# Kernel optimization log

Hardware: AMD Instinct MI355X
Metric: run time of the kernel (lower is better)

Reference implementation:

```python
import jax, jax.numpy as jnp
import numpy as np

IN_SIZE = 784
Z_DIM = 128
K_DIM = 8192
BATCH = 16384
ENC_HIDDEN = [512, 256]          # EncoderMLP default
DEC_SIZES = [Z_DIM, 256, 512, 784]  # DecoderMLP default: [latent, *hidden]


def _linear(x, w, b):
    return x @ w + b


def find_nearest(query, target):
    # Faithful to: sqrt(sum((Q-T)^2, -1)).min(1)[1]; sqrt is monotone so
    # argmin of squared distance is identical. Computed via the GEMM
    # expansion instead of materializing the (N,K,D) broadcast tensor.
    q2 = jnp.sum(query * query, axis=1, keepdims=True)        # [N,1]
    t2 = jnp.sum(target * target, axis=1)                     # [K]
    d2 = q2 - 2.0 * (query @ target.T) + t2[None, :]          # [N,K]
    idx = jnp.argmin(d2, axis=1)
    return target[idx]


def setup_inputs() -> dict:
    key = jax.random.key(0)
    ks = jax.random.split(key, 16)
    s = 0.02
    inp = {"X": jax.random.uniform(ks[0], (BATCH, 1, 28, 28), dtype=jnp.float32)}
    # Encoder: 784 -> 512 -> 256 (mlp blocks, ReLU) -> 128 (plain Linear)
    enc_sizes = [IN_SIZE] + ENC_HIDDEN + [Z_DIM]
    for i, (din, dout) in enumerate(zip(enc_sizes, enc_sizes[1:]), 1):
        inp[f"enc_w{i}"] = s * jax.random.normal(ks[i], (din, dout), dtype=jnp.float32)
        inp[f"enc_b{i}"] = jnp.zeros((dout,), dtype=jnp.float32)
    # Codebook
    inp["codebook"] = jax.random.normal(ks[8], (K_DIM, Z_DIM), dtype=jnp.float32)
    # Decoder: 128 -> 256 -> 512 -> 784 (mlp blocks, ReLU) + sigmoid out
    for i, (din, dout) in enumerate(zip(DEC_SIZES, DEC_SIZES[1:]), 1):
        inp[f"dec_w{i}"] = s * jax.random.normal(ks[8 + i], (din, dout), dtype=jnp.float32)
        inp[f"dec_b{i}"] = jnp.zeros((dout,), dtype=jnp.float32)
    return inp


def reference(X, enc_w1, enc_b1, enc_w2, enc_b2, enc_w3, enc_b3, codebook,
              dec_w1, dec_b1, dec_w2, dec_b2, dec_w3, dec_b3):
    x = X.reshape(-1, IN_SIZE)
    # Encoder (mlp_block = Linear+ReLU, final layer plain Linear)
    h = jax.nn.relu(_linear(x, enc_w1, enc_b1))
    h = jax.nn.relu(_linear(h, enc_w2, enc_b2))
    z_enc = _linear(h, enc_w3, enc_b3)                         # [N, Z]
    # Nearest codebook vector for each encoding
    z_dec = find_nearest(z_enc, codebook)                      # [N, Z]
    # Decoder
    d = jax.nn.relu(_linear(z_dec, dec_w1, dec_b1))
    d = jax.nn.relu(_linear(d, dec_w2, dec_b2))
    d = jax.nn.relu(_linear(d, dec_w3, dec_b3))
    x_recon = jax.nn.sigmoid(d).reshape(-1, 1, 28, 28)
    # Nearest encoding for each codebook vector (for embedding loss)
    z_enc_for_embd = find_nearest(codebook, z_enc)             # [K, Z]
    return (x_recon, z_enc, z_dec, z_enc_for_embd)
```

## Files before the change

kernel.cpp:

```cpp
#include <hip/hip_runtime.h>
#include <math.h>

using u16 = unsigned short;
using u32 = unsigned int;
using u64 = unsigned long long;

typedef __bf16 bf16x8 __attribute__((ext_vector_type(8)));
typedef short  s16x8  __attribute__((ext_vector_type(8)));
typedef float  f32x4  __attribute__((ext_vector_type(4)));

__device__ __forceinline__ float b2f(u16 u){
  union { u32 i; float f; } x; x.i = ((u32)u) << 16; return x.f;
}
__device__ __forceinline__ u16 f2b(float f){
  union { float f; u32 i; } x; x.f = f;
  u32 i = x.i;
  u32 r = (i + 0x7fffu + ((i >> 16) & 1u)) >> 16;
  return (u16)r;
}
__device__ __forceinline__ f32x4 mfma16(s16x8 a, s16x8 b, f32x4 c){
  return __builtin_amdgcn_mfma_f32_16x16x32_bf16(
      __builtin_bit_cast(bf16x8, a), __builtin_bit_cast(bf16x8, b), c, 0, 0, 0);
}
__device__ __forceinline__ u64 shfl_xor_u64(u64 v, int m){
  int lo = __shfl_xor((int)(u32)v, m);
  int hi = __shfl_xor((int)(u32)(v >> 32), m);
  return ((u64)(u32)hi << 32) | (u32)lo;
}
__device__ __forceinline__ u64 umin64(u64 a, u64 b){ return a < b ? a : b; }
__device__ __forceinline__ u64 packmin(float v, int idx){
  u32 b = __float_as_uint(v);
  b = (b & 0x80000000u) ? ~b : (b | 0x80000000u);
  return ((u64)b << 32) | (u32)idx;
}
__device__ __forceinline__ void gload16(const void* g, void* l){
  __builtin_amdgcn_global_load_lds(
      (const __attribute__((address_space(1))) unsigned int*)g,
      (__attribute__((address_space(3))) unsigned int*)l, 16, 0, 0);
}

__global__ __launch_bounds__(256) void canary_k(float* out, float code){
  out[threadIdx.x] = code;
}

__global__ __launch_bounds__(256) void prep_weights(
    const float* __restrict__ w1, const float* __restrict__ w2, const float* __restrict__ w3,
    const float* __restrict__ dw1, const float* __restrict__ dw2, const float* __restrict__ dw3,
    const float* __restrict__ cb,
    u16* __restrict__ o1h, u16* __restrict__ o1l, u16* __restrict__ o2h, u16* __restrict__ o2l,
    u16* __restrict__ o3h, u16* __restrict__ o3l, u16* __restrict__ o4h, u16* __restrict__ o4l,
    u16* __restrict__ o5h, u16* __restrict__ o5l, u16* __restrict__ o6h, u16* __restrict__ o6l,
    u16* __restrict__ cbh, u16* __restrict__ cbl)
{
  size_t o = (size_t)blockIdx.x * 256 + threadIdx.x;
  if (o >= 1155072){
    size_t e = o - 1155072;
    if (e >= 1048576) return;
    float v = cb[e];
    u16 h = f2b(v);
    cbh[e] = h;
    cbl[e] = f2b(v - b2f(h));
    return;
  }
  const float* src; u16 *hi, *lo; int K, N, Kp; size_t base;
  if      (o <  425984){ src=w1;  hi=o1h; lo=o1l; K=784; N=512; Kp=832; base=0; }
  else if (o <  557056){ src=w2;  hi=o2h; lo=o2l; K=512; N=256; Kp=512; base=425984; }
  else if (o <  589824){ src=w3;  hi=o3h; lo=o3l; K=256; N=128; Kp=256; base=557056; }
  else if (o <  622592){ src=dw1; hi=o4h; lo=o4l; K=128; N=256; Kp=128; base=589824; }
  else if (o <  753664){ src=dw2; hi=o5h; lo=o5l; K=256; N=512; Kp=256; base=622592; }
  else                 { src=dw3; hi=o6h; lo=o6l; K=512; N=784; Kp=512; base=753664; }
  size_t e = o - base;
  int n = (int)(e / Kp), kp = (int)(e % Kp);
  u16 h = 0, l = 0;
  if (kp < K){
    float v = src[(size_t)kp * N + n];
    h = f2b(v);
    l = f2b(v - b2f(h));
  }
  hi[e] = h; lo[e] = l;
}

__device__ __forceinline__ void norm_row(const float* __restrict__ src, float* __restrict__ dst){
  const float4* r = (const float4*)src;
  float s = 0.f;
  for (int k = 0; k < 32; k++){
    float4 p = r[k];
    s += p.x * p.x + p.y * p.y + p.z * p.z + p.w * p.w;
  }
  *dst = s;
}

struct __align__(16) SmemGemm {
  u16 Ah[128][72];
  u16 Al[128][72];
  u16 Bh[128][72];
  u16 Bl[128][72];
};

template<int ACT, int OUTP>
__device__ __forceinline__ void gemm_body(
    SmemGemm& sm,
    const float* __restrict__ A, const u16* __restrict__ B0, const u16* __restrict__ B1,
    const float* __restrict__ bias, float* __restrict__ Cf,
    u16* __restrict__ P0, u16* __restrict__ P1,
    int Astr, int KLIM, int Kp, int KT, int N, int nRowsB, int bx, int by)
{
  const int tid = threadIdx.x;
  const int m0 = by * 128, n0 = bx * 128;
  const int wave = tid >> 6, lane = tid & 63;
  const int wm = (wave >> 1) * 64, wn = (wave & 1) * 64;
  const int quad = lane >> 4, l15 = lane & 15;
  f32x4 acc[4][4] = {};

  for (int kt = 0; kt < KT; ++kt){
    const int kb = kt * 64;
    #pragma unroll
    for (int c = 0; c < 8; c++){
      int idx = c * 256 + tid;
      int r = idx >> 4, c4 = (idx & 15) * 4;
      float4 v = make_float4(0.f, 0.f, 0.f, 0.f);
      if (kb + c4 < KLIM)
        v = *(const float4*)(A + (size_t)(m0 + r) * Astr + kb + c4);
      ushort4 h, l;
      h.x = f2b(v.x); l.x = f2b(v.x - b2f(h.x));
      h.y = f2b(v.y); l.y = f2b(v.y - b2f(h.y));
      h.z = f2b(v.z); l.z = f2b(v.z - b2f(h.z));
      h.w = f2b(v.w); l.w = f2b(v.w - b2f(h.w));
      *(ushort4*)&sm.Ah[r][c4] = h;
      *(ushort4*)&sm.Al[r][c4] = l;
    }
    #pragma unroll
    for (int c = 0; c < 4; c++){
      int idx = c * 256 + tid;
      int r = idx >> 3, col = (idx & 7) * 8;
      int rb = n0 + r; rb = rb < nRowsB ? rb : nRowsB - 1;
      *(uint4*)&sm.Bh[r][col] = *(const uint4*)(B0 + (size_t)rb * Kp + kb + col);
      *(uint4*)&sm.Bl[r][col] = *(const uint4*)(B1 + (size_t)rb * Kp + kb + col);
    }
    __syncthreads();
    #pragma unroll
    for (int kh = 0; kh < 2; ++kh){
      s16x8 ah[4], al[4], bh[4], bl[4];
      #pragma unroll
      for (int t4 = 0; t4 < 4; t4++){
        ah[t4] = *(const s16x8*)&sm.Ah[wm + t4 * 16 + l15][kh * 32 + quad * 8];
        al[t4] = *(const s16x8*)&sm.Al[wm + t4 * 16 + l15][kh * 32 + quad * 8];
        bh[t4] = *(const s16x8*)&sm.Bh[wn + t4 * 16 + l15][kh * 32 + quad * 8];
        bl[t4] = *(const s16x8*)&sm.Bl[wn + t4 * 16 + l15][kh * 32 + quad * 8];
      }
      #pragma unroll
      for (int mt = 0; mt < 4; mt++)
        #pragma unroll
        for (int nt = 0; nt < 4; nt++){
          acc[mt][nt] = mfma16(ah[mt], bh[nt], acc[mt][nt]);
          acc[mt][nt] = mfma16(ah[mt], bl[nt], acc[mt][nt]);
          acc[mt][nt] = mfma16(al[mt], bh[nt], acc[mt][nt]);
        }
    }
    __syncthreads();
  }

  float bvs[4]; int cols[4];
  #pragma unroll
  for (int nt = 0; nt < 4; nt++){
    int cN = n0 + wn + nt * 16 + l15;
    cols[nt] = cN;
    int cc = cN < N ? cN : N - 1;
    bvs[nt] = bias[cc];
  }
  #pragma unroll
  for (int mt = 0; mt < 4; mt++){
    int rbase = m0 + wm + mt * 16 + quad * 4;
    #pragma unroll
    for (int nt = 0; nt < 4; nt++){
      if (cols[nt] < N){
        #pragma unroll
        for (int r = 0; r < 4; r++){
          float v = acc[mt][nt][r] + bvs[nt];
          if (ACT >= 1) v = v > 0.f ? v : 0.f;
          if (ACT == 2) v = 1.f / (1.f + expf(-v));
          size_t off = (size_t)(rbase + r) * N + cols[nt];
          if (OUTP == 2){
            P0[off] = f2b(v);
          } else {
            Cf[off] = v;
            if (OUTP == 1){
              u16 h = f2b(v);
              P0[off] = h;
              P1[off] = f2b(v - b2f(h));
            }
          }
        }
      }
    }
  }
}

template<int ACT, int OUTP>
__global__ __launch_bounds__(256, 2) void gemm_k(
    const float* __restrict__ A, const u16* __restrict__ B0, const u16* __restrict__ B1,
    const float* __restrict__ bias, float* __restrict__ Cf,
    u16* __restrict__ P0, u16* __restrict__ P1,
    int Astr, int KLIM, int Kp, int KT, int N, int nRowsB)
{
  __shared__ SmemGemm sm;
  gemm_body<ACT, OUTP>(sm, A, B0, B1, bias, Cf, P0, P1, Astr, KLIM, Kp, KT, N, nRowsB,
                       blockIdx.x, blockIdx.y);
}

__global__ __launch_bounds__(256, 2) void fused1(
    const float* __restrict__ X,  const u16* __restrict__ W1h, const u16* __restrict__ W1l,
    const float* __restrict__ b1, float* __restrict__ h1,
    const float* __restrict__ cb, const u16* __restrict__ D1h, const u16* __restrict__ D1l,
    const float* __restrict__ db1, float* __restrict__ g1, float* __restrict__ t2f)
{
  __shared__ SmemGemm sm;
  int bid = blockIdx.x;
  if (bid < 512){
    gemm_body<1,0>(sm, X, W1h, W1l, b1, h1, nullptr, nullptr, 784, 784, 832, 13, 512, 512,
                   bid & 3, bid >> 2);
  } else if (bid < 640){
    int b = bid - 512;
    gemm_body<1,0>(sm, cb, D1h, D1l, db1, g1, nullptr, nullptr, 128, 128, 128, 2, 256, 256,
                   b & 1, b >> 1);
  } else {
    int r = (bid - 640) * 256 + threadIdx.x;
    norm_row(cb + (size_t)r * 128, t2f + r);
  }
}

__global__ __launch_bounds__(256, 2) void fused2(
    const float* __restrict__ h1, const u16* __restrict__ W2h, const u16* __restrict__ W2l,
    const float* __restrict__ b2, float* __restrict__ h2,
    const float* __restrict__ g1, const u16* __restrict__ D2h, const u16* __restrict__ D2l,
    const float* __restrict__ db2, float* __restrict__ g2)
{
  __shared__ SmemGemm sm;
  int bid = blockIdx.x;
  if (bid < 256){
    gemm_body<1,0>(sm, h1, W2h, W2l, b2, h2, nullptr, nullptr, 512, 512, 512, 8, 256, 256,
                   bid & 1, bid >> 1);
  } else {
    int b = bid - 256;
    gemm_body<1,0>(sm, g1, D2h, D2l, db2, g2, nullptr, nullptr, 256, 256, 256, 4, 512, 512,
                   b & 3, b >> 2);
  }
}

struct __align__(16) DistSmem {
  u16 smem[2][16384];
  u64 colbuf[4][128];
  u64 sRow[2][128];
  float q2s[128];
};

__device__ __forceinline__ void dist_body(
    DistSmem& sm,
    const u16* __restrict__ Zh, const u16* __restrict__ Zl,
    const u16* __restrict__ Bh, const u16* __restrict__ Bl,
    const float* __restrict__ zenc, const float* __restrict__ t2,
    u64* __restrict__ rowp, u64* __restrict__ colp, int strip, int iblk)
{
  const int tid = threadIdx.x;
  const int i0 = iblk * 128;
  const int wave = tid >> 6, lane = tid & 63;
  const int wm = (wave >> 1) * 32, wn = (wave & 1) * 64;
  const int quad = lane >> 4, l15 = lane & 15;

  const int swz = (l15 & 7) << 4;
  const int cof0 = (((quad << 4)     ) ^ swz) >> 1;
  const int cof1 = (((quad << 4) | 64) ^ swz) >> 1;

  if (tid < 128){
    norm_row(zenc + (size_t)(i0 + tid) * 128, &sm.q2s[tid]);
  }

  s16x8 zh[2][2][2], zl[2][2][2];
  #pragma unroll
  for (int kb = 0; kb < 2; kb++)
    #pragma unroll
    for (int kh = 0; kh < 2; kh++)
      #pragma unroll
      for (int mt = 0; mt < 2; mt++){
        size_t off = (size_t)(i0 + wm + mt * 16 + l15) * 128 + kb * 64 + kh * 32 + quad * 8;
        zh[kb][kh][mt] = *(const s16x8*)(Zh + off);
        zl[kb][kh][mt] = *(const s16x8*)(Zl + off);
      }

  #define STAGE(jt_, kb_, buf_) {                                              \
    size_t jb = (size_t)(strip * 2048 + (jt_) * 128) * 128 + (kb_) * 64;       \
    _Pragma("unroll")                                                          \
    for (int c = 0; c < 2; c++){                                               \
      int ci = c * 512 + tid;                                                  \
      int row = ci >> 3;                                                       \
      size_t g = jb + (size_t)row * 128 + (size_t)(((ci & 7) ^ (row & 7)) * 8);\
      u16* lp = &sm.smem[buf_][ci * 8];                                        \
      gload16(Bh + g, lp);                                                     \
      gload16(Bl + g, lp + 8192);                                              \
    }                                                                          \
  }

  #define COMPUTE(buf_, kb_) {                                                 \
    __builtin_amdgcn_s_setprio(1);                                             \
    _Pragma("unroll")                                                          \
    for (int kh = 0; kh < 2; kh++){                                            \
      const int cof = kh ? cof1 : cof0;                                        \
      s16x8 bh[4], bl[4];                                                      \
      _Pragma("unroll")                                                        \
      for (int nt = 0; nt < 4; nt++){                                          \
        int off = (wn + nt * 16 + l15) * 64 + cof;                             \
        bh[nt] = *(const s16x8*)&sm.smem[buf_][off];                           \
        bl[nt] = *(const s16x8*)&sm.smem[buf_][8192 + off];                    \
      }                                                                        \
      _Pragma("unroll")                                                        \
      for (int mt = 0; mt < 2; mt++)                                           \
        _Pragma("unroll")                                                      \
        for (int nt = 0; nt < 4; nt++){                                        \
          acc[mt][nt] = mfma16(zh[kb_][kh][mt], bh[nt], acc[mt][nt]);          \
          acc[mt][nt] = mfma16(zh[kb_][kh][mt], bl[nt], acc[mt][nt]);          \
          acc[mt][nt] = mfma16(zl[kb_][kh][mt], bh[nt], acc[mt][nt]);          \
          acc[mt][nt] = mfma16(zl[kb_][kh][mt], bl[nt], acc[mt][nt]);          \
        }                                                                      \
    }                                                                          \
    __builtin_amdgcn_s_setprio(0);                                             \
  }

  STAGE(0, 0, 0);

  asm volatile("s_waitcnt lgkmcnt(0)" ::: "memory");
  __builtin_amdgcn_s_barrier();

  float qv[2][4];
  #pragma unroll
  for (int mt = 0; mt < 2; mt++)
    #pragma unroll
    for (int r = 0; r < 4; r++)
      qv[mt][r] = sm.q2s[wm + mt * 16 + quad * 4 + r];

  u64 rowm[2][4];
  #pragma unroll
  for (int mt = 0; mt < 2; mt++)
    #pragma unroll
    for (int r = 0; r < 4; r++) rowm[mt][r] = ~0ULL;

  #pragma unroll 1
  for (int jt = 0; jt < 16; ++jt){
    const int j0 = strip * 2048 + jt * 128;
    float t2v[4]; int gj[4];
    #pragma unroll
    for (int nt = 0; nt < 4; nt++){
      gj[nt] = j0 + wn + nt * 16 + l15;
      t2v[nt] = t2[gj[nt]];
    }
    f32x4 acc[2][4] = {};

    STAGE(jt, 1, 1);
    asm volatile("s_waitcnt vmcnt(8)" ::: "memory");
    __builtin_amdgcn_s_barrier();
    COMPUTE(0, 0)
    __builtin_amdgcn_s_barrier();
    if (jt < 15){
      STAGE(jt + 1, 0, 0);
      asm volatile("s_waitcnt vmcnt(4)" ::: "memory");
    } else {
      asm volatile("s_waitcnt vmcnt(0)" ::: "memory");
    }
    __builtin_amdgcn_s_barrier();
    COMPUTE(1, 1)

    #pragma unroll
    for (int mt = 0; mt < 2; mt++){
      #pragma unroll
      for (int r = 0; r < 4; r++){
        float qq = qv[mt][r];
        float rbest = (qq - 2.f * acc[mt][0][r]) + t2v[0];
        int   ridx  = gj[0];
        #pragma unroll
        for (int nt = 1; nt < 4; nt++){
          float v = (qq - 2.f * acc[mt][nt][r]) + t2v[nt];
          if (v < rbest){ rbest = v; ridx = gj[nt]; }
        }
        rowm[mt][r] = umin64(rowm[mt][r], packmin(rbest, ridx));
      }
    }
    #pragma unroll
    for (int nt = 0; nt < 4; nt++){
      float cbest = 3.4e38f; int cidx = 0;
      #pragma unroll
      for (int mt = 0; mt < 2; mt++){
        #pragma unroll
        for (int r = 0; r < 4; r++){
          float vc = (t2v[nt] - 2.f * acc[mt][nt][r]) + qv[mt][r];
          if (vc < cbest){ cbest = vc; cidx = i0 + wm + mt * 16 + quad * 4 + r; }
        }
      }
      u64 p = packmin(cbest, cidx);
      p = umin64(p, shfl_xor_u64(p, 16));
      p = umin64(p, shfl_xor_u64(p, 32));
      if (quad == 0)
        sm.colbuf[wave >> 1][wn + nt * 16 + l15] = p;
    }
    __builtin_amdgcn_s_barrier();
    if (tid < 128){
      u64 p = umin64(umin64(sm.colbuf[0][tid], sm.colbuf[1][tid]),
                     umin64(sm.colbuf[2][tid], sm.colbuf[3][tid]));
      colp[(size_t)iblk * 8192 + j0 + tid] = p;
    }
  }
  #undef STAGE
  #undef COMPUTE

  #pragma unroll
  for (int mt = 0; mt < 2; mt++)
    #pragma unroll
    for (int r = 0; r < 4; r++){
      u64 p = rowm[mt][r];
      p = umin64(p, shfl_xor_u64(p, 1));
      p = umin64(p, shfl_xor_u64(p, 2));
      p = umin64(p, shfl_xor_u64(p, 4));
      p = umin64(p, shfl_xor_u64(p, 8));
      rowm[mt][r] = p;
    }
  if (l15 == 0){
    #pragma unroll
    for (int mt = 0; mt < 2; mt++)
      #pragma unroll
      for (int r = 0; r < 4; r++)
        sm.sRow[wave & 1][wm + mt * 16 + quad * 4 + r] = rowm[mt][r];
  }
  __syncthreads();
  if (tid < 128)
    rowp[(size_t)strip * 16384 + i0 + tid] = umin64(sm.sRow[0][tid], sm.sRow[1][tid]);
}

union SmemF4 { SmemGemm g; DistSmem d; };

__global__ __launch_bounds__(512, 2) void fused_dd(
    const u16* __restrict__ Zh, const u16* __restrict__ Zl,
    const u16* __restrict__ Bh, const u16* __restrict__ Bl,
    const float* __restrict__ zenc, const float* __restrict__ t2,
    u64* __restrict__ rowp, u64* __restrict__ colp,
    const float* __restrict__ g2, const u16* __restrict__ D3h, const u16* __restrict__ D3l,
    const float* __restrict__ db3, u16* __restrict__ xdecb)
{
  __shared__ SmemF4 sm;
  int bid = blockIdx.x;
  if (bid < 512){
    dist_body(sm.d, Zh, Zl, Bh, Bl, zenc, t2, rowp, colp, bid & 3, bid >> 2);
  } else {
    if (threadIdx.x >= 256) return;
    int b = bid - 512;
    gemm_body<2,2>(sm.g, g2, D3h, D3l, db3, nullptr, xdecb, nullptr,
                   512, 512, 512, 8, 784, 784, b % 7, b / 7);
  }
}

__global__ __launch_bounds__(256) void reduce_rc(
    const u64* __restrict__ rowp, const u64* __restrict__ colp,
    const float* __restrict__ cb, const float* __restrict__ zenc,
    float* __restrict__ zdec, float* __restrict__ zembd, int* __restrict__ rowidx)
{
  int tid = threadIdx.x;
  __shared__ u64 s[4][64];
  __shared__ int sidx[64];
  if (blockIdx.x < 256){
    int base = blockIdx.x * 64;
    int n = base + (tid & 63);
    u64 best = ~0ULL;
    for (int p = tid >> 6; p < 4; p += 4)
      best = umin64(best, rowp[(size_t)p * 16384 + n]);
    s[tid >> 6][tid & 63] = best;
    __syncthreads();
    if (tid < 64){
      u64 b = umin64(umin64(s[0][tid], s[1][tid]), umin64(s[2][tid], s[3][tid]));
      int idx = (int)(b & 0xffffffffULL);
      idx = idx < 0 ? 0 : (idx > 8191 ? 8191 : idx);
      sidx[tid] = idx;
      rowidx[base + tid] = idx;
    }
    __syncthreads();
    for (int q = 0; q < 32; q++){
      int e = q * 256 + tid; int r = e >> 7, c = e & 127;
      zdec[(size_t)(base + r) * 128 + c] = cb[(size_t)sidx[r] * 128 + c];
    }
  } else {
    int base = (blockIdx.x - 256) * 64;
    int n = base + (tid & 63);
    u64 best = ~0ULL;
    for (int p = tid >> 6; p < 128; p += 4)
      best = umin64(best, colp[(size_t)p * 8192 + n]);
    s[tid >> 6][tid & 63] = best;
    __syncthreads();
    if (tid < 64){
      u64 b = umin64(umin64(s[0][tid], s[1][tid]), umin64(s[2][tid], s[3][tid]));
      int idx = (int)(b & 0xffffffffULL);
      idx = idx < 0 ? 0 : (idx > 16383 ? 16383 : idx);
      sidx[tid] = idx;
    }
    __syncthreads();
    for (int q = 0; q < 32; q++){
      int e = q * 256 + tid; int r = e >> 7, c = e & 127;
      zembd[(size_t)(base + r) * 128 + c] = zenc[(size_t)sidx[r] * 128 + c];
    }
  }
}

__global__ __launch_bounds__(256) void gather_xrec(
    const u16* __restrict__ xdecb, const int* __restrict__ rowidx, float* __restrict__ xrec)
{
  size_t o = (size_t)blockIdx.x * 256 + threadIdx.x;
  int row = (int)(o / 784), c = (int)(o % 784);
  int idx = rowidx[row];
  idx = idx < 0 ? 0 : (idx > 8191 ? 8191 : idx);
  xrec[o] = b2f(xdecb[(size_t)idx * 784 + c]);
}

extern "C" void kernel_launch(void* const* d_in, const int* in_sizes, int n_in,
                              void* d_out, int out_size, void* d_ws, size_t ws_size,
                              hipStream_t stream){
  const float* X   = (const float*)d_in[0];
  const float* w1  = (const float*)d_in[1];  const float* b1  = (const float*)d_in[2];
  const float* w2  = (const float*)d_in[3];  const float* b2  = (const float*)d_in[4];
  const float* w3  = (const float*)d_in[5];  const float* b3  = (const float*)d_in[6];
  const float* cb  = (const float*)d_in[7];
  const float* dw1 = (const float*)d_in[8];  const float* db1 = (const float*)d_in[9];
  const float* dw2 = (const float*)d_in[10]; const float* db2 = (const float*)d_in[11];
  const float* dw3 = (const float*)d_in[12]; const float* db3 = (const float*)d_in[13];

  float* out   = (float*)d_out;
  float* xrec  = out;
  float* zenc  = out + 12845056;
  float* zdec  = zenc + 2097152;
  float* zembd = zdec + 2097152;

  const size_t NEEDED = 22020096;
  if (ws_size < NEEDED){
    canary_k<<<1, 256, 0, stream>>>(out, 1000.0f + (float)(ws_size >> 20));
    return;
  }

  char* ob = (char*)d_out;
  float* h1   = (float*)(ob + 0);
  float* g1   = (float*)(ob + 33554432);
  u16*   zhi  = (u16*)(ob + 33554432);
  u16*   zlo  = (u16*)(ob + 37748736);
  u16*   cbhi = (u16*)(ob + 41943040);
  u16*   cblo = (u16*)(ob + 44040192);
  u64*   colp = (u64*)(ob + 0);
  float* g2   = (float*)(ob + 55574528);

  char* w = (char*)d_ws;
  u16* W1Th = (u16*)(w + 0);        u16* W1Tl = (u16*)(w + 851968);
  u16* W2Th = (u16*)(w + 1703936);  u16* W2Tl = (u16*)(w + 1966080);
  u16* W3Th = (u16*)(w + 2228224);  u16* W3Tl = (u16*)(w + 2293760);
  u16* D1Th = (u16*)(w + 2359296);  u16* D1Tl = (u16*)(w + 2424832);
  u16* D2Th = (u16*)(w + 2490368);  u16* D2Tl = (u16*)(w + 2752512);
  u16* D3Th = (u16*)(w + 3014656);  u16* D3Tl = (u16*)(w + 3817472);
  float* t2f = (float*)(w + 4620288);
  int*  rowi = (int*)(w + 4653056);
  u64*  rowp = (u64*)(w + 4718592);
  float* h2  = (float*)(w + 5242880);
  u16* xdecb = (u16*)(w + 5242880);

  prep_weights<<<8608, 256, 0, stream>>>(w1, w2, w3, dw1, dw2, dw3, cb,
      W1Th, W1Tl, W2Th, W2Tl, W3Th, W3Tl, D1Th, D1Tl, D2Th, D2Tl, D3Th, D3Tl, cbhi, cblo);

  fused1<<<672, 256, 0, stream>>>(X, W1Th, W1Tl, b1, h1, cb, D1Th, D1Tl, db1, g1, t2f);

  fused2<<<512, 256, 0, stream>>>(h1, W2Th, W2Tl, b2, h2, g1, D2Th, D2Tl, db2, g2);

  gemm_k<0, 1><<<dim3(1, 128), 256, 0, stream>>>(h2, W3Th, W3Tl, b3, zenc, zhi, zlo,
                                                 256, 256, 256, 4, 128, 128);

  fused_dd<<<960, 512, 0, stream>>>(zhi, zlo, cbhi, cblo, zenc, t2f, rowp, colp,
                                    g2, D3Th, D3Tl, db3, xdecb);

  reduce_rc<<<384, 256, 0, stream>>>(rowp, colp, cb, zenc, zdec, zembd, rowi);

  gather_xrec<<<50176, 256, 0, stream>>>(xdecb, rowi, xrec);
}
```

Measured before the change: 504.9 us.

## Regroup co-scheduled kernels: fuse enc layer3 with dec layer2, decoder layer3 with reductions

Reorganizes which independent stages share a launch. Encoder layer 2 now runs alone. Encoder layer 3 is co-launched with decoder layer 2, and the distance kernel runs on its own. The final decoder GEMM is co-launched with the row/col argmin reductions. Scratch buffers move to avoid overlap in the output region. The aim is to balance work per launch and cut the idle tail from mixing heavy and light block types, but the kernel count stays the same and the dependencies shift.

```diff
diff --git a/kernel.cpp b/kernel.cpp
--- a/kernel.cpp
+++ b/kernel.cpp
@@ -229,19 +229,20 @@
   }
 }
 
-__global__ __launch_bounds__(256, 2) void fused2(
-    const float* __restrict__ h1, const u16* __restrict__ W2h, const u16* __restrict__ W2l,
-    const float* __restrict__ b2, float* __restrict__ h2,
+__global__ __launch_bounds__(256, 2) void fused3(
+    const float* __restrict__ h2, const u16* __restrict__ W3h, const u16* __restrict__ W3l,
+    const float* __restrict__ b3, float* __restrict__ zenc,
+    u16* __restrict__ zhi, u16* __restrict__ zlo,
     const float* __restrict__ g1, const u16* __restrict__ D2h, const u16* __restrict__ D2l,
     const float* __restrict__ db2, float* __restrict__ g2)
 {
   __shared__ SmemGemm sm;
   int bid = blockIdx.x;
-  if (bid < 256){
-    gemm_body<1,0>(sm, h1, W2h, W2l, b2, h2, nullptr, nullptr, 512, 512, 512, 8, 256, 256,
-                   bid & 1, bid >> 1);
+  if (bid < 128){
+    gemm_body<0,1>(sm, h2, W3h, W3l, b3, zenc, zhi, zlo, 256, 256, 256, 4, 128, 128,
+                   0, bid);
   } else {
-    int b = bid - 256;
+    int b = bid - 128;
     gemm_body<1,0>(sm, g1, D2h, D2l, db2, g2, nullptr, nullptr, 256, 256, 256, 4, 512, 512,
                    b & 3, b >> 2);
   }
@@ -433,74 +434,77 @@
     rowp[(size_t)strip * 16384 + i0 + tid] = umin64(sm.sRow[0][tid], sm.sRow[1][tid]);
 }
 
-union SmemF4 { SmemGemm g; DistSmem d; };
-
-__global__ __launch_bounds__(512, 2) void fused_dd(
+__global__ __launch_bounds__(512, 2) void dist_k(
     const u16* __restrict__ Zh, const u16* __restrict__ Zl,
     const u16* __restrict__ Bh, const u16* __restrict__ Bl,
     const float* __restrict__ zenc, const float* __restrict__ t2,
-    u64* __restrict__ rowp, u64* __restrict__ colp,
+    u64* __restrict__ rowp, u64* __restrict__ colp)
+{
+  __shared__ DistSmem sm;
+  dist_body(sm, Zh, Zl, Bh, Bl, zenc, t2, rowp, colp, blockIdx.x & 3, blockIdx.x >> 2);
+}
+
+union SmemF5 {
+  SmemGemm g;
+  struct { u64 s[4][64]; int sidx[64]; } r;
+};
+
+__global__ __launch_bounds__(256, 2) void fused5(
     const float* __restrict__ g2, const u16* __restrict__ D3h, const u16* __restrict__ D3l,
-    const float* __restrict__ db3, u16* __restrict__ xdecb)
-{
-  __shared__ SmemF4 sm;
-  int bid = blockIdx.x;
-  if (bid < 512){
-    dist_body(sm.d, Zh, Zl, Bh, Bl, zenc, t2, rowp, colp, bid & 3, bid >> 2);
-  } else {
-    if (threadIdx.x >= 256) return;
-    int b = bid - 512;
-    gemm_body<2,2>(sm.g, g2, D3h, D3l, db3, nullptr, xdecb, nullptr,
-                   512, 512, 512, 8, 784, 784, b % 7, b / 7);
-  }
-}
-
-__global__ __launch_bounds__(256) void reduce_rc(
+    const float* __restrict__ db3, u16* __restrict__ xdecb,
     const u64* __restrict__ rowp, const u64* __restrict__ colp,
     const float* __restrict__ cb, const float* __restrict__ zenc,
     float* __restrict__ zdec, float* __restrict__ zembd, int* __restrict__ rowidx)
 {
+  __shared__ SmemF5 sm;
+  int bid = blockIdx.x;
+  if (bid < 448){
+    gemm_body<2,2>(sm.g, g2, D3h, D3l, db3, nullptr, xdecb, nullptr,
+                   512, 512, 512, 8, 784, 784, bid % 7, bid / 7);
+    return;
+  }
+  bid -= 448;
   int tid = threadIdx.x;
-  __shared__ u64 s[4][64];
-  __shared__ int sidx[64];
-  if (blockIdx.x < 256){
-    int base = blockIdx.x * 64;
+  if (bid < 256){
+    int base = bid * 64;
     int n = base + (tid & 63);
     u64 best = ~0ULL;
     for (int p = tid >> 6; p < 4; p += 4)
       best = umin64(best, rowp[(size_t)p * 16384 + n]);
-    s[tid >> 6][tid & 63] = best;
+    sm.r.s[tid >> 6][tid & 63] = best;
     __syncthreads();
     if (tid < 64){
-      u64 b = umin64(umin64(s[0][tid], s[1][tid]), umin64(s[2][tid], s[3][tid]));
+      u64 b = umin64(umin64(sm.r.s[0][tid], sm.r.s[1][tid]),
+                     umin64(sm.r.s[2][tid], sm.r.s[3][tid]));
       int idx = (int)(b & 0xffffffffULL);
       idx = idx < 0 ? 0 : (idx > 8191 ? 8191 : idx);
-      sidx[tid] = idx;
+      sm.r.sidx[tid] = idx;
       rowidx[base + tid] = idx;
     }
     __syncthreads();
     for (int q = 0; q < 32; q++){
       int e = q * 256 + tid; int r = e >> 7, c = e & 127;
-      zdec[(size_t)(base + r) * 128 + c] = cb[(size_t)sidx[r] * 128 + c];
+      zdec[(size_t)(base + r) * 128 + c] = cb[(size_t)sm.r.sidx[r] * 128 + c];
     }
   } else {
-    int base = (blockIdx.x - 256) * 64;
+    int base = (bid - 256) * 64;
     int n = base + (tid & 63);
     u64 best = ~0ULL;
     for (int p = tid >> 6; p < 128; p += 4)
       best = umin64(best, colp[(size_t)p * 8192 + n]);
-    s[tid >> 6][tid & 63] = best;
+    sm.r.s[tid >> 6][tid & 63] = best;
     __syncthreads();
     if (tid < 64){
-      u64 b = umin64(umin64(s[0][tid], s[1][tid]), umin64(s[2][tid], s[3][tid]));
+      u64 b = umin64(umin64(sm.r.s[0][tid], sm.r.s[1][tid]),
+                     umin64(sm.r.s[2][tid], sm.r.s[3][tid]));
       int idx = (int)(b & 0xffffffffULL);
       idx = idx < 0 ? 0 : (idx > 16383 ? 16383 : idx);
-      sidx[tid] = idx;
+      sm.r.sidx[tid] = idx;
     }
     __syncthreads();
     for (int q = 0; q < 32; q++){
       int e = q * 256 + tid; int r = e >> 7, c = e & 127;
-      zembd[(size_t)(base + r) * 128 + c] = zenc[(size_t)sidx[r] * 128 + c];
+      zembd[(size_t)(base + r) * 128 + c] = zenc[(size_t)sm.r.sidx[r] * 128 + c];
     }
   }
 }
@@ -541,13 +545,13 @@
 
   char* ob = (char*)d_out;
   float* h1   = (float*)(ob + 0);
+  u16*   zhi  = (u16*)(ob + 8388608);
+  u16*   zlo  = (u16*)(ob + 12582912);
+  float* g2   = (float*)(ob + 16777216);
   float* g1   = (float*)(ob + 33554432);
-  u16*   zhi  = (u16*)(ob + 33554432);
-  u16*   zlo  = (u16*)(ob + 37748736);
   u16*   cbhi = (u16*)(ob + 41943040);
   u16*   cblo = (u16*)(ob + 44040192);
   u64*   colp = (u64*)(ob + 0);
-  float* g2   = (float*)(ob + 55574528);
 
   char* w = (char*)d_ws;
   u16* W1Th = (u16*)(w + 0);        u16* W1Tl = (u16*)(w + 851968);
@@ -567,15 +571,16 @@
 
   fused1<<<672, 256, 0, stream>>>(X, W1Th, W1Tl, b1, h1, cb, D1Th, D1Tl, db1, g1, t2f);
 
-  fused2<<<512, 256, 0, stream>>>(h1, W2Th, W2Tl, b2, h2, g1, D2Th, D2Tl, db2, g2);
-
-  gemm_k<0, 1><<<dim3(1, 128), 256, 0, stream>>>(h2, W3Th, W3Tl, b3, zenc, zhi, zlo,
-                                                 256, 256, 256, 4, 128, 128);
-
-  fused_dd<<<960, 512, 0, stream>>>(zhi, zlo, cbhi, cblo, zenc, t2f, rowp, colp,
-                                    g2, D3Th, D3Tl, db3, xdecb);
-
-  reduce_rc<<<384, 256, 0, stream>>>(rowp, colp, cb, zenc, zdec, zembd, rowi);
+  gemm_k<1, 0><<<dim3(2, 128), 256, 0, stream>>>(h1, W2Th, W2Tl, b2, h2, nullptr, nullptr,
+                                                 512, 512, 512, 8, 256, 256);
+
+  fused3<<<384, 256, 0, stream>>>(h2, W3Th, W3Tl, b3, zenc, zhi, zlo,
+                                  g1, D2Th, D2Tl, db2, g2);
+
+  dist_k<<<512, 512, 0, stream>>>(zhi, zlo, cbhi, cblo, zenc, t2f, rowp, colp);
+
+  fused5<<<832, 256, 0, stream>>>(g2, D3Th, D3Tl, db3, xdecb,
+                                  rowp, colp, cb, zenc, zdec, zembd, rowi);
 
   gather_xrec<<<50176, 256, 0, stream>>>(xdecb, rowi, xrec);
 }
```

New measurement: 500.1 us. Within noise of the previous version (-0.9%).
